# Optimization experiments

Measured on AMD Instinct MI355X. Metric: run time of the kernel, lower is better.

## Reference

```python
import jax, jax.numpy as jnp
import numpy as np


def setup_inputs() -> dict:
    key = jax.random.key(0)
    kq, kk, kv = jax.random.split(key, 3)
    L, D = 8192, 64
    return {
        "q": jax.random.normal(kq, (L, D), dtype=jnp.float32),
        "k": jax.random.normal(kk, (L, D), dtype=jnp.float32),
        "v": jax.random.normal(kv, (L, D), dtype=jnp.float32),
    }


def reference(q, k, v):
    # score = q @ k^T  (NOTE: source applies no 1/sqrt(d) scaling)
    score = jnp.einsum("qd,kd->qk", q, k)          # [Lq, Lk]
    score = jax.nn.softmax(score, axis=-1)          # row-wise softmax
    out = jnp.einsum("qk,kd->qd", score, v)         # [Lq, D]
    return (out, score)
```

## Files before the change

kernel.cpp:

```cpp
#include <hip/hip_runtime.h>

#define LSEQ 8192
#define DDIM 64
#define SHIFT 20.0f
#define QTILE 64
#define KC 64

#define KSPL1 16
#define KRANGE1 (LSEQ / KSPL1)
#define KSPL2 8
#define KRANGE2 (LSEQ / KSPL2)

#define VSTR 72
#define PSTR 72

typedef __attribute__((ext_vector_type(8))) short bf16x8;
typedef __attribute__((ext_vector_type(4))) float f32x4;

#define MFMA16(a, b, c) __builtin_amdgcn_mfma_f32_16x16x32_bf16(a, b, c, 0, 0, 0)

__device__ inline short f2bf(float x) {
    unsigned u = __float_as_uint(x);
    u += 0x7FFF + ((u >> 16) & 1);
    return (short)(u >> 16);
}

__device__ inline void split8(float4 a, float4 b, bf16x8& hi, bf16x8& lo) {
    float t[8] = {a.x, a.y, a.z, a.w, b.x, b.y, b.z, b.w};
#pragma unroll
    for (int j = 0; j < 8; ++j) {
        unsigned u  = __float_as_uint(t[j]);
        unsigned hu = u & 0xFFFF0000u;
        hi[j] = (short)(hu >> 16);
        lo[j] = f2bf(t[j] - __uint_as_float(hu));
    }
}

#define QK_TILE(acc, R)                                                             \
    {                                                                               \
        const int   sw  = ((R) & 7) << 4;                                           \
        const char* khb = KhiB + (R) * 128;                                         \
        const char* klb = KloB + (R) * 128;                                         \
        bf16x8 khi0 = *(const bf16x8*)(khb + ((quad * 16) ^ sw));                   \
        bf16x8 khi1 = *(const bf16x8*)(khb + ((64 + quad * 16) ^ sw));              \
        bf16x8 klo0 = *(const bf16x8*)(klb + ((quad * 16) ^ sw));                   \
        bf16x8 klo1 = *(const bf16x8*)(klb + ((64 + quad * 16) ^ sw));              \
        acc = MFMA16(qhi0, khi0, acc);                                              \
        acc = MFMA16(qhi1, khi1, acc);                                              \
        acc = MFMA16(qlo0, khi0, acc);                                              \
        acc = MFMA16(qlo1, khi1, acc);                                              \
        acc = MFMA16(qhi0, klo0, acc);                                              \
        acc = MFMA16(qhi1, klo1, acc);                                              \
    }

#define K_ISSUE(kc_)                                                                \
    { _Pragma("unroll") for (int ii = 0; ii < 2; ++ii) {                            \
        int s = ii * 256 + tid; int kk = s >> 3, dseg = s & 7;                      \
        const float* kp = kptr + (size_t)(kb + (kc_) + kk) * DDIM + dseg * 8;       \
        pk0[ii] = *(const float4*)kp; pk1[ii] = *(const float4*)(kp + 4); } }

#define K_COMMIT()                                                                  \
    { _Pragma("unroll") for (int ii = 0; ii < 2; ++ii) {                            \
        int s = ii * 256 + tid; int kk = s >> 3, dseg = s & 7;                      \
        bf16x8 hi, lo; split8(pk0[ii], pk1[ii], hi, lo);                            \
        int off = kk * 128 + ((dseg * 16) ^ ((kk & 7) << 4));                       \
        *(bf16x8*)(KhiB + off) = hi; *(bf16x8*)(KloB + off) = lo; } }

#define V_ISSUE(kc_)                                                                \
    { _Pragma("unroll") for (int ii = 0; ii < 4; ++ii) {                            \
        int e4 = (ii * 256 + tid) * 4; int d = e4 & 63, kl2 = e4 >> 6;              \
        pv[ii] = *(const float4*)(vptr + (size_t)(kb + (kc_) + kl2) * DDIM + d); } }

#define V_COMMIT()                                                                  \
    { _Pragma("unroll") for (int ii = 0; ii < 4; ++ii) {                            \
        int e4 = (ii * 256 + tid) * 4; int d = e4 & 63, kl2 = e4 >> 6;              \
        VT[(d + 0) * VSTR + kl2] = (unsigned short)f2bf(pv[ii].x);                  \
        VT[(d + 1) * VSTR + kl2] = (unsigned short)f2bf(pv[ii].y);                  \
        VT[(d + 2) * VSTR + kl2] = (unsigned short)f2bf(pv[ii].z);                  \
        VT[(d + 3) * VSTR + kl2] = (unsigned short)f2bf(pv[ii].w); } }

#define Q_FRAGS(qrow)                                                               \
    {                                                                               \
        const float* qp = q + (size_t)(qrow) * DDIM;                                \
        float4 a = *(const float4*)(qp + quad * 8);                                 \
        float4 b = *(const float4*)(qp + quad * 8 + 4);                             \
        split8(a, b, qhi0, qlo0);                                                   \
        a = *(const float4*)(qp + 32 + quad * 8);                                   \
        b = *(const float4*)(qp + 32 + quad * 8 + 4);                               \
        split8(a, b, qhi1, qlo1);                                                   \
    }

__global__ __launch_bounds__(256, 4) void sdpa_rowsum(
    const float* __restrict__ q, const float* __restrict__ k, float* __restrict__ l)
{
    const int tid = threadIdx.x, lane = tid & 63, wave = tid >> 6;
    const int quad = lane >> 4, r = lane & 15;
    const int q0 = blockIdx.x * QTILE, kb = blockIdx.y * KRANGE1;
    const float* kptr = k;

    __shared__ __align__(16) char KhiS[KC * 128];
    __shared__ __align__(16) char KloS[KC * 128];
    char* KhiB = KhiS; char* KloB = KloS;

    bf16x8 qhi0, qlo0, qhi1, qlo1;
    Q_FRAGS(q0 + wave * 16 + r);

    float4 pk0[2], pk1[2];
    K_ISSUE(0);
    K_COMMIT();
    __syncthreads();

    float esum[4] = {0.f, 0.f, 0.f, 0.f};

    for (int kc = 0; kc < KRANGE1; kc += KC) {
        const bool more = (kc + KC) < KRANGE1;
        if (more) K_ISSUE(kc + KC);
#pragma unroll
        for (int kt = 0; kt < KC / 16; ++kt) {
            const int R = kt * 16 + r;
            f32x4 acc = {0.f, 0.f, 0.f, 0.f};
            QK_TILE(acc, R);
#pragma unroll
            for (int i = 0; i < 4; ++i) esum[i] += __expf(acc[i] - SHIFT);
        }
        __syncthreads();
        if (more) K_COMMIT();
        __syncthreads();
    }
#pragma unroll
    for (int i = 0; i < 4; ++i) {
#pragma unroll
        for (int off = 1; off < 16; off <<= 1) esum[i] += __shfl_xor(esum[i], off);
    }
    if (r == 0) {
#pragma unroll
        for (int i = 0; i < 4; ++i)
            atomicAdd(&l[q0 + wave * 16 + quad * 4 + i], esum[i]);
    }
}

__global__ __launch_bounds__(256, 4) void sdpa_score_pv(
    const float* __restrict__ q, const float* __restrict__ k, const float* __restrict__ v,
    const float* __restrict__ l, float* __restrict__ outp, float* __restrict__ score)
{
    const int tid = threadIdx.x, lane = tid & 63, wave = tid >> 6;
    const int quad = lane >> 4, r = lane & 15;
    const int q0 = blockIdx.x * QTILE, kb = blockIdx.y * KRANGE2;
    const float* kptr = k;
    const float* vptr = v;

    __shared__ __align__(16) char KhiS[KC * 128];
    __shared__ __align__(16) char KloS[KC * 128];
    __shared__ __align__(16) unsigned short VT[DDIM * VSTR];
    __shared__ __align__(16) unsigned short PL[4][16 * PSTR];
    char* KhiB = KhiS; char* KloB = KloS;

    bf16x8 qhi0, qlo0, qhi1, qlo1;
    Q_FRAGS(q0 + wave * 16 + r);

    float  lr[4];
    size_t rowbase[4];
#pragma unroll
    for (int i = 0; i < 4; ++i) {
        int qrow   = q0 + wave * 16 + quad * 4 + i;
        lr[i]      = 1.0f / l[qrow];
        rowbase[i] = (size_t)qrow * LSEQ + kb;
    }

    unsigned short* Pl = PL[wave];
    f32x4 accpv[4];
#pragma unroll
    for (int nb = 0; nb < 4; ++nb) accpv[nb] = (f32x4){0.f, 0.f, 0.f, 0.f};

    float4 pk0[2], pk1[2], pv[4];
    K_ISSUE(0);
    V_ISSUE(0);
    K_COMMIT();
    V_COMMIT();
    __syncthreads();

    for (int kc = 0; kc < KRANGE2; kc += KC) {
        const bool more = (kc + KC) < KRANGE2;
        if (more) { K_ISSUE(kc + KC); V_ISSUE(kc + KC); }

#pragma unroll
        for (int kt = 0; kt < KC / 16; ++kt) {
            const int R = kt * 16 + r;
            f32x4 acc = {0.f, 0.f, 0.f, 0.f};
            QK_TILE(acc, R);
#pragma unroll
            for (int i = 0; i < 4; ++i) {
                float p = __expf(acc[i] - SHIFT) * lr[i];
                __builtin_nontemporal_store(p, &score[rowbase[i] + kc + kt * 16 + r]);
                Pl[(quad * 4 + i) * PSTR + kt * 16 + r] = (unsigned short)f2bf(p);
            }
        }
#pragma unroll
        for (int ks = 0; ks < 2; ++ks) {
            bf16x8 afrag = *(const bf16x8*)(&Pl[r * PSTR + ks * 32 + quad * 8]);
#pragma unroll
            for (int nb = 0; nb < 4; ++nb) {
                bf16x8 bfrag = *(const bf16x8*)(&VT[(nb * 16 + r) * VSTR + ks * 32 + quad * 8]);
                accpv[nb] = MFMA16(afrag, bfrag, accpv[nb]);
            }
        }
        __syncthreads();
        if (more) { K_COMMIT(); V_COMMIT(); }
        __syncthreads();
    }

#pragma unroll
    for (int nb = 0; nb < 4; ++nb) {
#pragma unroll
        for (int i = 0; i < 4; ++i) {
            int qrow = q0 + wave * 16 + quad * 4 + i;
            atomicAdd(&outp[(size_t)qrow * DDIM + nb * 16 + r], accpv[nb][i]);
        }
    }
}

extern "C" void kernel_launch(void* const* d_in, const int* in_sizes, int n_in,
                              void* d_out, int out_size, void* d_ws, size_t ws_size,
                              hipStream_t stream) {
    const float* q = (const float*)d_in[0];
    const float* k = (const float*)d_in[1];
    const float* v = (const float*)d_in[2];
    float* out   = (float*)d_out;
    float* score = out + (size_t)LSEQ * DDIM;
    float* l     = (float*)d_ws;

    hipMemsetAsync(l, 0, LSEQ * sizeof(float), stream);
    hipMemsetAsync(out, 0, (size_t)LSEQ * DDIM * sizeof(float), stream);

    sdpa_rowsum  <<<dim3(LSEQ / QTILE, KSPL1), 256, 0, stream>>>(q, k, l);
    sdpa_score_pv<<<dim3(LSEQ / QTILE, KSPL2), 256, 0, stream>>>(q, k, v, l, out, score);
}
```

Measured before the change: 430.0 us.

## Double-buffer K/V tiles, widen Q tile to 128, add setprio

```diff
diff --git a/kernel.cpp b/kernel.cpp
--- a/kernel.cpp
+++ b/kernel.cpp
@@ -3,7 +3,7 @@
 #define LSEQ 8192
 #define DDIM 64
 #define SHIFT 20.0f
-#define QTILE 64
+#define QTILE 128
 #define KC 64
 
 #define KSPL1 16
@@ -12,7 +12,7 @@
 #define KRANGE2 (LSEQ / KSPL2)
 
 #define VSTR 72
-#define PSTR 72
+#define PSTR 68
 
 typedef __attribute__((ext_vector_type(8))) short bf16x8;
 typedef __attribute__((ext_vector_type(4))) float f32x4;
@@ -36,59 +36,58 @@
     }
 }
 
-#define QK_TILE(acc, R)                                                             \
+#define QK_TILE(acc, khB, klB, R)                                                   \
     {                                                                               \
         const int   sw  = ((R) & 7) << 4;                                           \
-        const char* khb = KhiB + (R) * 128;                                         \
-        const char* klb = KloB + (R) * 128;                                         \
-        bf16x8 khi0 = *(const bf16x8*)(khb + ((quad * 16) ^ sw));                   \
-        bf16x8 khi1 = *(const bf16x8*)(khb + ((64 + quad * 16) ^ sw));              \
-        bf16x8 klo0 = *(const bf16x8*)(klb + ((quad * 16) ^ sw));                   \
-        bf16x8 klo1 = *(const bf16x8*)(klb + ((64 + quad * 16) ^ sw));              \
-        acc = MFMA16(qhi0, khi0, acc);                                              \
-        acc = MFMA16(qhi1, khi1, acc);                                              \
-        acc = MFMA16(qlo0, khi0, acc);                                              \
-        acc = MFMA16(qlo1, khi1, acc);                                              \
-        acc = MFMA16(qhi0, klo0, acc);                                              \
-        acc = MFMA16(qhi1, klo1, acc);                                              \
+        const char* khb = (khB) + (R) * 128;                                        \
+        const char* klb = (klB) + (R) * 128;                                        \
+        bf16x8 kh0 = *(const bf16x8*)(khb + ((quad * 16) ^ sw));                    \
+        bf16x8 kh1 = *(const bf16x8*)(khb + ((64 + quad * 16) ^ sw));               \
+        bf16x8 kl0 = *(const bf16x8*)(klb + ((quad * 16) ^ sw));                    \
+        bf16x8 kl1 = *(const bf16x8*)(klb + ((64 + quad * 16) ^ sw));               \
+        acc = MFMA16(qh[s][0], kh0, acc);                                           \
+        acc = MFMA16(qh[s][1], kh1, acc);                                           \
+        acc = MFMA16(ql[s][0], kh0, acc);                                           \
+        acc = MFMA16(ql[s][1], kh1, acc);                                           \
+        acc = MFMA16(qh[s][0], kl0, acc);                                           \
+        acc = MFMA16(qh[s][1], kl1, acc);                                           \
     }
 
 #define K_ISSUE(kc_)                                                                \
     { _Pragma("unroll") for (int ii = 0; ii < 2; ++ii) {                            \
-        int s = ii * 256 + tid; int kk = s >> 3, dseg = s & 7;                      \
+        int s_ = ii * 256 + tid; int kk = s_ >> 3, dseg = s_ & 7;                   \
         const float* kp = kptr + (size_t)(kb + (kc_) + kk) * DDIM + dseg * 8;       \
         pk0[ii] = *(const float4*)kp; pk1[ii] = *(const float4*)(kp + 4); } }
 
-#define K_COMMIT()                                                                  \
+#define K_COMMIT(khB, klB)                                                          \
     { _Pragma("unroll") for (int ii = 0; ii < 2; ++ii) {                            \
-        int s = ii * 256 + tid; int kk = s >> 3, dseg = s & 7;                      \
+        int s_ = ii * 256 + tid; int kk = s_ >> 3, dseg = s_ & 7;                   \
         bf16x8 hi, lo; split8(pk0[ii], pk1[ii], hi, lo);                            \
         int off = kk * 128 + ((dseg * 16) ^ ((kk & 7) << 4));                       \
-        *(bf16x8*)(KhiB + off) = hi; *(bf16x8*)(KloB + off) = lo; } }
+        *(bf16x8*)((khB) + off) = hi; *(bf16x8*)((klB) + off) = lo; } }
 
 #define V_ISSUE(kc_)                                                                \
     { _Pragma("unroll") for (int ii = 0; ii < 4; ++ii) {                            \
         int e4 = (ii * 256 + tid) * 4; int d = e4 & 63, kl2 = e4 >> 6;              \
-        pv[ii] = *(const float4*)(vptr + (size_t)(kb + (kc_) + kl2) * DDIM + d); } }
-
-#define V_COMMIT()                                                                  \
+        pvv[ii] = *(const float4*)(vptr + (size_t)(kb + (kc_) + kl2) * DDIM + d); } }
+
+#define V_COMMIT(vtB)                                                               \
     { _Pragma("unroll") for (int ii = 0; ii < 4; ++ii) {                            \
         int e4 = (ii * 256 + tid) * 4; int d = e4 & 63, kl2 = e4 >> 6;              \
-        VT[(d + 0) * VSTR + kl2] = (unsigned short)f2bf(pv[ii].x);                  \
-        VT[(d + 1) * VSTR + kl2] = (unsigned short)f2bf(pv[ii].y);                  \
-        VT[(d + 2) * VSTR + kl2] = (unsigned short)f2bf(pv[ii].z);                  \
-        VT[(d + 3) * VSTR + kl2] = (unsigned short)f2bf(pv[ii].w); } }
-
-#define Q_FRAGS(qrow)                                                               \
-    {                                                                               \
-        const float* qp = q + (size_t)(qrow) * DDIM;                                \
+        (vtB)[(d + 0) * VSTR + kl2] = (unsigned short)f2bf(pvv[ii].x);              \
+        (vtB)[(d + 1) * VSTR + kl2] = (unsigned short)f2bf(pvv[ii].y);              \
+        (vtB)[(d + 2) * VSTR + kl2] = (unsigned short)f2bf(pvv[ii].z);              \
+        (vtB)[(d + 3) * VSTR + kl2] = (unsigned short)f2bf(pvv[ii].w); } }
+
+#define Q_FRAGS()                                                                   \
+    { _Pragma("unroll") for (int s = 0; s < 2; ++s) {                               \
+        const float* qp = q + (size_t)(q0 + wave * 32 + s * 16 + r) * DDIM;         \
         float4 a = *(const float4*)(qp + quad * 8);                                 \
         float4 b = *(const float4*)(qp + quad * 8 + 4);                             \
-        split8(a, b, qhi0, qlo0);                                                   \
+        split8(a, b, qh[s][0], ql[s][0]);                                           \
         a = *(const float4*)(qp + 32 + quad * 8);                                   \
         b = *(const float4*)(qp + 32 + quad * 8 + 4);                               \
-        split8(a, b, qhi1, qlo1);                                                   \
-    }
+        split8(a, b, qh[s][1], ql[s][1]); } }
 
 __global__ __launch_bounds__(256, 4) void sdpa_rowsum(
     const float* __restrict__ q, const float* __restrict__ k, float* __restrict__ l)
@@ -98,48 +97,64 @@
     const int q0 = blockIdx.x * QTILE, kb = blockIdx.y * KRANGE1;
     const float* kptr = k;
 
-    __shared__ __align__(16) char KhiS[KC * 128];
-    __shared__ __align__(16) char KloS[KC * 128];
-    char* KhiB = KhiS; char* KloB = KloS;
-
-    bf16x8 qhi0, qlo0, qhi1, qlo1;
-    Q_FRAGS(q0 + wave * 16 + r);
+    __shared__ __align__(16) char KhiS[2][KC * 128];
+    __shared__ __align__(16) char KloS[2][KC * 128];
+
+    bf16x8 qh[2][2], ql[2][2];
+    Q_FRAGS();
 
     float4 pk0[2], pk1[2];
     K_ISSUE(0);
-    K_COMMIT();
+    K_COMMIT(KhiS[0], KloS[0]);
+    K_ISSUE(KC);
     __syncthreads();
 
-    float esum[4] = {0.f, 0.f, 0.f, 0.f};
-
-    for (int kc = 0; kc < KRANGE1; kc += KC) {
-        const bool more = (kc + KC) < KRANGE1;
-        if (more) K_ISSUE(kc + KC);
-#pragma unroll
-        for (int kt = 0; kt < KC / 16; ++kt) {
-            const int R = kt * 16 + r;
-            f32x4 acc = {0.f, 0.f, 0.f, 0.f};
-            QK_TILE(acc, R);
-#pragma unroll
-            for (int i = 0; i < 4; ++i) esum[i] += __expf(acc[i] - SHIFT);
-        }
+    float esum[2][4];
+#pragma unroll
+    for (int s = 0; s < 2; ++s)
+#pragma unroll
+        for (int i = 0; i < 4; ++i) esum[s][i] = 0.f;
+
+    const int NCH = KRANGE1 / KC;
+    for (int c = 0; c < NCH; ++c) {
+        const char* khB = KhiS[c & 1];
+        const char* klB = KloS[c & 1];
+        __builtin_amdgcn_s_setprio(1);
+#pragma unroll
+        for (int s = 0; s < 2; ++s) {
+#pragma unroll
+            for (int kt = 0; kt < KC / 16; ++kt) {
+                const int R = kt * 16 + r;
+                f32x4 acc = {0.f, 0.f, 0.f, 0.f};
+                QK_TILE(acc, khB, klB, R);
+#pragma unroll
+                for (int i = 0; i < 4; ++i) esum[s][i] += __expf(acc[i] - SHIFT);
+            }
+        }
+        __builtin_amdgcn_s_setprio(0);
+        if (c + 1 < NCH) K_COMMIT(KhiS[(c + 1) & 1], KloS[(c + 1) & 1]);
+        if (c + 2 < NCH) K_ISSUE((c + 2) * KC);
         __syncthreads();
-        if (more) K_COMMIT();
-        __syncthreads();
-    }
-#pragma unroll
-    for (int i = 0; i < 4; ++i) {
-#pragma unroll
-        for (int off = 1; off < 16; off <<= 1) esum[i] += __shfl_xor(esum[i], off);
-    }
+    }
+
+#pragma unroll
+    for (int s = 0; s < 2; ++s)
+#pragma unroll
+        for (int i = 0; i < 4; ++i) {
+#pragma unroll
+            for (int off = 1; off < 16; off <<= 1)
+                esum[s][i] += __shfl_xor(esum[s][i], off);
+        }
     if (r == 0) {
 #pragma unroll
-        for (int i = 0; i < 4; ++i)
-            atomicAdd(&l[q0 + wave * 16 + quad * 4 + i], esum[i]);
-    }
-}
-
-__global__ __launch_bounds__(256, 4) void sdpa_score_pv(
+        for (int s = 0; s < 2; ++s)
+#pragma unroll
+            for (int i = 0; i < 4; ++i)
+                atomicAdd(&l[q0 + wave * 32 + s * 16 + quad * 4 + i], esum[s][i]);
+    }
+}
+
+__global__ __launch_bounds__(256, 2) void sdpa_score_pv(
     const float* __restrict__ q, const float* __restrict__ k, const float* __restrict__ v,
     const float* __restrict__ l, float* __restrict__ outp, float* __restrict__ score)
 {
@@ -149,74 +164,95 @@
     const float* kptr = k;
     const float* vptr = v;
 
-    __shared__ __align__(16) char KhiS[KC * 128];
-    __shared__ __align__(16) char KloS[KC * 128];
-    __shared__ __align__(16) unsigned short VT[DDIM * VSTR];
-    __shared__ __align__(16) unsigned short PL[4][16 * PSTR];
-    char* KhiB = KhiS; char* KloB = KloS;
-
-    bf16x8 qhi0, qlo0, qhi1, qlo1;
-    Q_FRAGS(q0 + wave * 16 + r);
-
-    float  lr[4];
-    size_t rowbase[4];
-#pragma unroll
-    for (int i = 0; i < 4; ++i) {
-        int qrow   = q0 + wave * 16 + quad * 4 + i;
-        lr[i]      = 1.0f / l[qrow];
-        rowbase[i] = (size_t)qrow * LSEQ + kb;
-    }
-
-    unsigned short* Pl = PL[wave];
-    f32x4 accpv[4];
-#pragma unroll
-    for (int nb = 0; nb < 4; ++nb) accpv[nb] = (f32x4){0.f, 0.f, 0.f, 0.f};
-
-    float4 pk0[2], pk1[2], pv[4];
+    __shared__ __align__(16) char KhiS[2][KC * 128];
+    __shared__ __align__(16) char KloS[2][KC * 128];
+    __shared__ __align__(16) unsigned short VTS[2][DDIM * VSTR];
+    __shared__ __align__(16) unsigned short PLS[4][32 * PSTR];
+
+    bf16x8 qh[2][2], ql[2][2];
+    Q_FRAGS();
+
+    float  lr[2][4];
+    size_t rowbase[2][4];
+#pragma unroll
+    for (int s = 0; s < 2; ++s)
+#pragma unroll
+        for (int i = 0; i < 4; ++i) {
+            int qrow      = q0 + wave * 32 + s * 16 + quad * 4 + i;
+            lr[s][i]      = 1.0f / l[qrow];
+            rowbase[s][i] = (size_t)qrow * LSEQ + kb;
+        }
+
+    unsigned short* Pl = PLS[wave];
+    f32x4 accpv[2][4];
+#pragma unroll
+    for (int s = 0; s < 2; ++s)
+#pragma unroll
+        for (int nb = 0; nb < 4; ++nb) accpv[s][nb] = (f32x4){0.f, 0.f, 0.f, 0.f};
+
+    float4 pk0[2], pk1[2], pvv[4];
     K_ISSUE(0);
     V_ISSUE(0);
-    K_COMMIT();
-    V_COMMIT();
+    K_COMMIT(KhiS[0], KloS[0]);
+    V_COMMIT(VTS[0]);
+    K_ISSUE(KC);
+    V_ISSUE(KC);
     __syncthreads();
 
-    for (int kc = 0; kc < KRANGE2; kc += KC) {
-        const bool more = (kc + KC) < KRANGE2;
-        if (more) { K_ISSUE(kc + KC); V_ISSUE(kc + KC); }
-
-#pragma unroll
-        for (int kt = 0; kt < KC / 16; ++kt) {
-            const int R = kt * 16 + r;
-            f32x4 acc = {0.f, 0.f, 0.f, 0.f};
-            QK_TILE(acc, R);
+    const int NCH = KRANGE2 / KC;
+    for (int c = 0; c < NCH; ++c) {
+        const int kc = c * KC;
+        const char* khB = KhiS[c & 1];
+        const char* klB = KloS[c & 1];
+        const unsigned short* vtB = VTS[c & 1];
+
+        __builtin_amdgcn_s_setprio(1);
+#pragma unroll
+        for (int s = 0; s < 2; ++s) {
+#pragma unroll
+            for (int kt = 0; kt < KC / 16; ++kt) {
+                const int R = kt * 16 + r;
+                f32x4 acc = {0.f, 0.f, 0.f, 0.f};
+                QK_TILE(acc, khB, klB, R);
+#pragma unroll
+                for (int i = 0; i < 4; ++i) {
+                    float p = __expf(acc[i] - SHIFT) * lr[s][i];
+                    __builtin_nontemporal_store(p, &score[rowbase[s][i] + kc + kt * 16 + r]);
+                    Pl[(s * 16 + quad * 4 + i) * PSTR + kt * 16 + r] = (unsigned short)f2bf(p);
+                }
+            }
+        }
+#pragma unroll
+        for (int s = 0; s < 2; ++s) {
+#pragma unroll
+            for (int ks = 0; ks < 2; ++ks) {
+                bf16x8 af = *(const bf16x8*)(&Pl[(s * 16 + r) * PSTR + ks * 32 + quad * 8]);
+#pragma unroll
+                for (int nb = 0; nb < 4; ++nb) {
+                    bf16x8 bf_ = *(const bf16x8*)(&vtB[(nb * 16 + r) * VSTR + ks * 32 + quad * 8]);
+                    accpv[s][nb] = MFMA16(af, bf_, accpv[s][nb]);
+                }
+            }
+        }
+        __builtin_amdgcn_s_setprio(0);
+
+        if (c + 1 < NCH) {
+            K_COMMIT(KhiS[(c + 1) & 1], KloS[(c + 1) & 1]);
+            V_COMMIT(VTS[(c + 1) & 1]);
+        }
+        if (c + 2 < NCH) { K_ISSUE((c + 2) * KC); V_ISSUE((c + 2) * KC); }
+        __syncthreads();
+    }
+
+#pragma unroll
+    for (int s = 0; s < 2; ++s)
+#pragma unroll
+        for (int nb = 0; nb < 4; ++nb)
 #pragma unroll
             for (int i = 0; i < 4; ++i) {
-                float p = __expf(acc[i] - SHIFT) * lr[i];
-                __builtin_nontemporal_store(p, &score[rowbase[i] + kc + kt * 16 + r]);
-                Pl[(quad * 4 + i) * PSTR + kt * 16 + r] = (unsigned short)f2bf(p);
-            }
-        }
-#pragma unroll
-        for (int ks = 0; ks < 2; ++ks) {
-            bf16x8 afrag = *(const bf16x8*)(&Pl[r * PSTR + ks * 32 + quad * 8]);
-#pragma unroll
-            for (int nb = 0; nb < 4; ++nb) {
-                bf16x8 bfrag = *(const bf16x8*)(&VT[(nb * 16 + r) * VSTR + ks * 32 + quad * 8]);
-                accpv[nb] = MFMA16(afrag, bfrag, accpv[nb]);
-            }
-        }
-        __syncthreads();
-        if (more) { K_COMMIT(); V_COMMIT(); }
-        __syncthreads();
-    }
-
-#pragma unroll
-    for (int nb = 0; nb < 4; ++nb) {
-#pragma unroll
-        for (int i = 0; i < 4; ++i) {
-            int qrow = q0 + wave * 16 + quad * 4 + i;
-            atomicAdd(&outp[(size_t)qrow * DDIM + nb * 16 + r], accpv[nb][i]);
-        }
-    }
+                int qrow = q0 + wave * 32 + s * 16 + quad * 4 + i;
+                atomicAdd(&outp[(size_t)qrow * DDIM + nb * 16 + r], accpv[s][nb][i]);
+            }
 }
 
 extern "C" void kernel_launch(void* const* d_in, const int* in_sizes, int n_in,
```

Result: faster. 403.8 us (-6.1%).
